# Performance work log

Hardware: AMD Instinct MI355X
Metric: run time of the kernel (lower is better)

The kernel has to match this reference:

```python
import jax, jax.numpy as jnp
import numpy as np
from jax import lax

B, N0, N1 = 4, 256, 256
NVOX = N0 * N1
NSUB, NLOR, RAYLEN, NTOF = 8, 32768, 256, 1
NBLK, CH = 4, 16
SUBSETS = np.linspace(0, NSUB, NBLK, endpoint=False).astype(int)  # [0,2,4,6]


def setup_inputs() -> dict:
    key = jax.random.key(0)
    ks = jax.random.split(key, 12)
    osem = jax.random.uniform(ks[0], (B, 1, N0, N1, 1), jnp.float32) + 0.1
    data = jax.random.uniform(ks[1], (B, NSUB, NLOR, NTOF), jnp.float32)
    mult = jax.random.uniform(ks[2], (B, NSUB, NLOR, 1), jnp.float32) + 0.5
    contam = jax.random.uniform(ks[3], (B, NSUB, NLOR, NTOF), jnp.float32) + 0.1
    adjoint_ones = jax.random.uniform(ks[4], (B, NSUB, N0, N1, 1), jnp.float32) + 0.5
    norm = jax.random.uniform(ks[5], (B,), jnp.float32) + 0.5
    ray_idx = jax.random.randint(ks[6], (NSUB, NLOR, RAYLEN), 0, NVOX, dtype=jnp.int32)
    proj_weights = jax.random.uniform(ks[7], (NSUB, NLOR, RAYLEN), jnp.float32) / RAYLEN
    w1 = jax.random.normal(ks[8], (CH, 1, 3, 3), jnp.float32) * 0.05
    b1 = jnp.zeros((CH,), jnp.float32)
    w2 = jax.random.normal(ks[9], (1, CH, 3, 3), jnp.float32) * 0.05
    b2 = jnp.zeros((1,), jnp.float32)
    net_weight = jnp.asarray(1.0, jnp.float32)
    return dict(osem=osem, data=data, multiplicative_corrections=mult,
                contamination=contam, adjoint_ones=adjoint_ones, norm=norm,
                ray_idx=ray_idx, proj_weights=proj_weights,
                w1=w1, b1=b1, w2=w2, b2=b2, net_weight=net_weight)


def _conv(x, w):
    return lax.conv_general_dilated(x, w, (1, 1), 'SAME',
                                    dimension_numbers=('NCHW', 'OIHW', 'NCHW'))


def _net(x, w1, b1, w2, b2):
    # x: (B,1,N0,N1,1) -> treat as NCHW 2D image with 1 channel
    img = x[:, :, :, :, 0]
    h = jax.nn.relu(_conv(img, w1) + b1[None, :, None, None])
    o = _conv(h, w2) + b2[None, :, None, None]
    return o[..., None]


def _fidelity(x, data, mult, contam, adj_ones, norm, ray_idx, pw, subset):
    # unscaled image, flattened: (B, NVOX)
    img_flat = norm[:, None] * x[:, 0, :, :, 0].reshape(B, NVOX)
    ii = ray_idx[subset]          # (NLOR, RAYLEN) voxel indices per ray
    ww = pw[subset]               # (NLOR, RAYLEN) Joseph weights
    # forward projection: gather + weighted sum along each ray
    fwd = jnp.einsum('bls,ls->bl', img_flat[:, ii], ww)[..., None]  # (B,NLOR,1)
    expected = mult[:, subset] * fwd + contam[:, subset]            # (B,NLOR,NTOF)
    ratio = (mult[:, subset] * (1.0 - data[:, subset] / expected)).sum(-1)  # (B,NLOR)
    # adjoint projection: scatter-add along each ray
    back = jnp.zeros((B, NVOX), x.dtype).at[:, ii].add(ww * ratio[:, :, None])
    upd = back * (img_flat / adj_ones[:, subset].reshape(B, NVOX))
    return (upd / norm[:, None]).reshape(B, 1, N0, N1, 1)


def reference(osem, data, multiplicative_corrections, contamination,
              adjoint_ones, norm, ray_idx, proj_weights,
              w1, b1, w2, b2, net_weight):
    x = osem
    for subset in SUBSETS:
        x_data = _fidelity(x, data, multiplicative_corrections, contamination,
                           adjoint_ones, norm, ray_idx, proj_weights, int(subset))
        x_net = _net(x, w1, b1, w2, b2)
        x = jax.nn.relu(osem - x_data + net_weight * x_net)
    return x
```

## Files before the change

kernel.cpp:

```cpp
#include <hip/hip_runtime.h>
#include <hip/hip_fp16.h>

#define BB 4
#define N0 256
#define N1 256
#define NVOX 65536
#define NSUB 8
#define NLOR 32768
#define RAYLEN 256
#define CH 16
#define NPTS (NLOR * RAYLEN)
#define VOXQ 16384
#define VOXT 32768

__global__ __launch_bounds__(256) void k_transpose(const float* __restrict__ osem,
                                                   float* __restrict__ xt) {
    int v = blockIdx.x * blockDim.x + threadIdx.x;
    if (v >= NVOX) return;
    float4 o;
    o.x = osem[0 * NVOX + v];
    o.y = osem[1 * NVOX + v];
    o.z = osem[2 * NVOX + v];
    o.w = osem[3 * NVOX + v];
    ((float4*)xt)[v] = o;
}

__global__ __launch_bounds__(256) void k_pack(const int* __restrict__ ridx,
                                              const float* __restrict__ pw,
                                              unsigned* __restrict__ packed) {
    int t = blockIdx.x * blockDim.x + threadIdx.x;
    int4   id = ((const int4*)ridx)[t];
    float4 w  = ((const float4*)pw)[t];
    uint4 o;
    o.x = (unsigned)id.x | ((unsigned)__half_as_ushort(__float2half_rn(w.x)) << 16);
    o.y = (unsigned)id.y | ((unsigned)__half_as_ushort(__float2half_rn(w.y)) << 16);
    o.z = (unsigned)id.z | ((unsigned)__half_as_ushort(__float2half_rn(w.z)) << 16);
    o.w = (unsigned)id.w | ((unsigned)__half_as_ushort(__float2half_rn(w.w)) << 16);
    ((uint4*)packed)[t] = o;
}

__device__ __forceinline__ float upk_w(unsigned p) {
    return __half2float(__ushort_as_half((unsigned short)(p >> 16)));
}

__device__ __forceinline__ unsigned pk2(float a, float b) {
    __half2 h = __floats2half2_rn(a, b);
    return *reinterpret_cast<unsigned*>(&h);
}

__global__ __launch_bounds__(256) void k_fwd_p(
    const unsigned* __restrict__ packed,
    const float* __restrict__ xt,
    const float* __restrict__ data,
    const float* __restrict__ mult,
    const float* __restrict__ contam,
    const float* __restrict__ norm,
    float* __restrict__ ratio)
{
    const int wave = threadIdx.x >> 6;
    const int lane = threadIdx.x & 63;
    const int l = blockIdx.x * 4 + wave;

    uint4 P = ((const uint4*)(packed + (size_t)l * RAYLEN))[lane];
    float ax = 0.f, ay = 0.f, az = 0.f, aw = 0.f;
    unsigned pp[4] = {P.x, P.y, P.z, P.w};
#pragma unroll
    for (int k = 0; k < 4; ++k) {
        float wt = upk_w(pp[k]);
        float4 xv = ((const float4*)xt)[pp[k] & 0xffffu];
        ax += xv.x * wt;
        ay += xv.y * wt;
        az += xv.z * wt;
        aw += xv.w * wt;
    }
#pragma unroll
    for (int off = 32; off >= 1; off >>= 1) {
        ax += __shfl_xor(ax, off);
        ay += __shfl_xor(ay, off);
        az += __shfl_xor(az, off);
        aw += __shfl_xor(aw, off);
    }
    if (lane == 0) {
        float fwd[4] = {ax, ay, az, aw};
        float rr[4];
#pragma unroll
        for (int b = 0; b < 4; ++b) {
            long o = (long)b * (NSUB * NLOR) + l;
            float m = mult[o];
            float e = m * (norm[b] * fwd[b]) + contam[o];
            rr[b] = m * (1.0f - data[o] / e);
        }
        ((float4*)ratio)[l] = make_float4(rr[0], rr[1], rr[2], rr[3]);
    }
}

__global__ __launch_bounds__(1024) void k_back_pk(
    const unsigned* __restrict__ packed,
    const float* __restrict__ ratio,
    unsigned* __restrict__ part,
    int PC)
{
    __shared__ unsigned acc[VOXQ];
    const int c = blockIdx.x;
    const int g = blockIdx.y;
    const int p = g & 1;
    const unsigned lo = (unsigned)(g >> 1) * VOXQ;

    for (int q = threadIdx.x; q < VOXQ; q += 1024) acc[q] = 0u;
    __syncthreads();

    const unsigned abase = (unsigned)(uintptr_t)(&acc[0]);

    const int n4 = PC >> 2;
    const uint4* src = (const uint4*)packed + (size_t)c * n4;
    const float2* rat2 = (const float2*)ratio;
    const int e0 = c * n4;

#define PKADD(u, R)                                                              \
    {                                                                            \
        unsigned q_ = ((u) & 0xffffu) - lo;                                      \
        if (q_ < VOXQ) {                                                         \
            float w_ = upk_w(u);                                                 \
            unsigned d_ = pk2(w_ * (R).x, w_ * (R).y);                           \
            unsigned a_ = abase + (q_ << 2);                                     \
            asm volatile("ds_pk_add_f16 %0, %1" :: "v"(a_), "v"(d_) : "memory"); \
        }                                                                        \
    }
#define PROC(P, R) PKADD(P.x, R) PKADD(P.y, R) PKADD(P.z, R) PKADD(P.w, R)

    for (int base4 = 0; base4 < n4; base4 += 4096) {
        const int ea = base4 + (int)threadIdx.x;
        uint4 A = src[ea];
        uint4 B = src[ea + 1024];
        uint4 C2 = src[ea + 2048];
        uint4 D = src[ea + 3072];
        float2 ra = rat2[(((e0 + ea) >> 6) << 1) + p];
        float2 rb = rat2[(((e0 + ea + 1024) >> 6) << 1) + p];
        float2 rc = rat2[(((e0 + ea + 2048) >> 6) << 1) + p];
        float2 rd = rat2[(((e0 + ea + 3072) >> 6) << 1) + p];
        PROC(A, ra) PROC(B, rb) PROC(C2, rc) PROC(D, rd)
    }
#undef PROC
#undef PKADD

    asm volatile("s_waitcnt lgkmcnt(0)" ::: "memory");
    __syncthreads();

    unsigned* dst = part + ((size_t)c * 2 + p) * NVOX + lo;
    for (int q = threadIdx.x; q < VOXQ; q += 1024) dst[q] = acc[q];
}

__global__ __launch_bounds__(256) void k_fwd(
    const int* __restrict__ ridx, const float* __restrict__ pw,
    const float* __restrict__ xt, const float* __restrict__ data,
    const float* __restrict__ mult, const float* __restrict__ contam,
    const float* __restrict__ norm, float* __restrict__ ratio)
{
    const int wave = threadIdx.x >> 6;
    const int lane = threadIdx.x & 63;
    const int l = blockIdx.x * 4 + wave;
    const long base = (long)l * RAYLEN;
    float ax = 0.f, ay = 0.f, az = 0.f, aw = 0.f;
#pragma unroll
    for (int k = 0; k < 4; ++k) {
        int r = lane + (k << 6);
        float wt = pw[base + r];
        float4 xv = ((const float4*)xt)[ridx[base + r]];
        ax += xv.x * wt; ay += xv.y * wt; az += xv.z * wt; aw += xv.w * wt;
    }
#pragma unroll
    for (int off = 32; off >= 1; off >>= 1) {
        ax += __shfl_xor(ax, off); ay += __shfl_xor(ay, off);
        az += __shfl_xor(az, off); aw += __shfl_xor(aw, off);
    }
    if (lane == 0) {
        float fwd[4] = {ax, ay, az, aw};
        float rr[4];
#pragma unroll
        for (int b = 0; b < 4; ++b) {
            long o = (long)b * (NSUB * NLOR) + l;
            float m = mult[o];
            float e = m * (norm[b] * fwd[b]) + contam[o];
            rr[b] = m * (1.0f - data[o] / e);
        }
        ((float4*)ratio)[l] = make_float4(rr[0], rr[1], rr[2], rr[3]);
    }
}

__global__ __launch_bounds__(1024) void k_back(
    const int* __restrict__ ridx, const float* __restrict__ pw,
    const float* __restrict__ ratio, float* __restrict__ part, int PC)
{
    __shared__ float acc[VOXT];
    const int c = blockIdx.x;
    const int g = blockIdx.y;
    const int b = g & 3;
    const int lo = (g >> 2) * VOXT;
    for (int q = threadIdx.x; q < VOXT; q += 1024) acc[q] = 0.0f;
    __syncthreads();
    const int pbeg = c * PC;
    const int pend = min(pbeg + PC, NPTS);
#pragma unroll 2
    for (int pt = pbeg + (int)threadIdx.x * 4; pt < pend; pt += 1024 * 4) {
        int4   id = *(const int4*)(ridx + pt);
        float4 w  = *(const float4*)(pw + pt);
        float  r  = ratio[(pt >> 8) * 4 + b];
        unsigned r0 = (unsigned)(id.x - lo), r1 = (unsigned)(id.y - lo);
        unsigned r2 = (unsigned)(id.z - lo), r3 = (unsigned)(id.w - lo);
        if (r0 < VOXT) atomicAdd(&acc[r0], w.x * r);
        if (r1 < VOXT) atomicAdd(&acc[r1], w.y * r);
        if (r2 < VOXT) atomicAdd(&acc[r2], w.z * r);
        if (r3 < VOXT) atomicAdd(&acc[r3], w.w * r);
    }
    __syncthreads();
    float4* dst = (float4*)(part + ((size_t)c * 4 + b) * NVOX + lo);
    const float4* srcl = (const float4*)acc;
    for (int q = threadIdx.x; q < VOXT / 4; q += 1024) dst[q] = srcl[q];
}

__global__ __launch_bounds__(256) void k_conv1(
    const float* __restrict__ xt,
    const float* __restrict__ w1,
    const float* __restrict__ b1,
    float* __restrict__ h)
{
    int t = blockIdx.x * blockDim.x + threadIdx.x;
    int b = t >> 16;
    int v = t & 65535;
    int i = v >> 8, j = v & 255;
    float in[3][3];
#pragma unroll
    for (int di = 0; di < 3; ++di)
#pragma unroll
        for (int dj = 0; dj < 3; ++dj) {
            int ii = i + di - 1, jj = j + dj - 1;
            in[di][dj] = (ii >= 0 && ii < N0 && jj >= 0 && jj < N1)
                             ? xt[(size_t)((ii << 8) | jj) * 4 + b]
                             : 0.0f;
        }
    float* hp = h + (size_t)t * CH;
#pragma unroll
    for (int c = 0; c < CH; ++c) {
        float acc = b1[c];
#pragma unroll
        for (int di = 0; di < 3; ++di)
#pragma unroll
            for (int dj = 0; dj < 3; ++dj)
                acc += in[di][dj] * w1[c * 9 + di * 3 + dj];
        hp[c] = fmaxf(acc, 0.0f);
    }
}

__global__ __launch_bounds__(256) void k_combine_pk(
    const float* __restrict__ h,
    const float* __restrict__ w2,
    const float* __restrict__ b2,
    const unsigned* __restrict__ part,
    const float* __restrict__ xt_in,
    const float* __restrict__ osem,
    const float* __restrict__ adj,
    const float* __restrict__ nwp,
    int C,
    float* __restrict__ xt_out,
    float* __restrict__ out_planar)
{
    int t = blockIdx.x * blockDim.x + threadIdx.x;
    int b = t >> 16;
    int v = t & 65535;
    int i = v >> 8, j = v & 255;

    float o = b2[0];
#pragma unroll
    for (int di = 0; di < 3; ++di) {
        int ii = i + di - 1;
        if (ii < 0 || ii >= N0) continue;
#pragma unroll
        for (int dj = 0; dj < 3; ++dj) {
            int jj = j + dj - 1;
            if (jj < 0 || jj >= N1) continue;
            const float* hp = h + ((size_t)b * NVOX + ((ii << 8) | jj)) * CH;
#pragma unroll
            for (int c = 0; c < CH; ++c)
                o += hp[c] * w2[c * 9 + di * 3 + dj];
        }
    }
    const int pr = b >> 1, hi = b & 1;
    float bk = 0.0f;
    for (int c = 0; c < C; ++c) {
        unsigned u = part[((size_t)c * 2 + pr) * NVOX + v];
        unsigned short us = hi ? (unsigned short)(u >> 16) : (unsigned short)(u & 0xffffu);
        bk += __half2float(__ushort_as_half(us));
    }

    float xv = xt_in[(size_t)v * 4 + b];
    float x_data = bk * xv / adj[(size_t)b * NSUB * NVOX + v];
    float xnew = osem[t] - x_data + nwp[0] * o;
    xnew = fmaxf(xnew, 0.0f);
    xt_out[(size_t)v * 4 + b] = xnew;
    if (out_planar) out_planar[t] = xnew;
}

__global__ __launch_bounds__(256) void k_combine(
    const float* __restrict__ h, const float* __restrict__ w2,
    const float* __restrict__ b2, const float* __restrict__ part,
    const float* __restrict__ xt_in, const float* __restrict__ osem,
    const float* __restrict__ adj, const float* __restrict__ nwp, int C,
    float* __restrict__ xt_out, float* __restrict__ out_planar)
{
    int t = blockIdx.x * blockDim.x + threadIdx.x;
    int b = t >> 16;
    int v = t & 65535;
    int i = v >> 8, j = v & 255;
    float o = b2[0];
#pragma unroll
    for (int di = 0; di < 3; ++di) {
        int ii = i + di - 1;
        if (ii < 0 || ii >= N0) continue;
#pragma unroll
        for (int dj = 0; dj < 3; ++dj) {
            int jj = j + dj - 1;
            if (jj < 0 || jj >= N1) continue;
            const float* hp = h + ((size_t)b * NVOX + ((ii << 8) | jj)) * CH;
#pragma unroll
            for (int c = 0; c < CH; ++c)
                o += hp[c] * w2[c * 9 + di * 3 + dj];
        }
    }
    float bk = 0.0f;
    for (int c = 0; c < C; ++c)
        bk += part[((size_t)c * 4 + b) * NVOX + v];
    float xv = xt_in[(size_t)v * 4 + b];
    float x_data = bk * xv / adj[(size_t)b * NSUB * NVOX + v];
    float xnew = osem[t] - x_data + nwp[0] * o;
    xnew = fmaxf(xnew, 0.0f);
    xt_out[(size_t)v * 4 + b] = xnew;
    if (out_planar) out_planar[t] = xnew;
}

extern "C" void kernel_launch(void* const* d_in, const int* in_sizes, int n_in,
                              void* d_out, int out_size, void* d_ws, size_t ws_size,
                              hipStream_t stream) {
    const float* osem   = (const float*)d_in[0];
    const float* data   = (const float*)d_in[1];
    const float* mult   = (const float*)d_in[2];
    const float* contam = (const float*)d_in[3];
    const float* adj    = (const float*)d_in[4];
    const float* norm   = (const float*)d_in[5];
    const int*   ray_idx = (const int*)d_in[6];
    const float* pw     = (const float*)d_in[7];
    const float* w1     = (const float*)d_in[8];
    const float* b1     = (const float*)d_in[9];
    const float* w2     = (const float*)d_in[10];
    const float* b2     = (const float*)d_in[11];
    const float* nw     = (const float*)d_in[12];
    float* out = (float*)d_out;

    const size_t MB = 1024 * 1024;
    float* ws  = (float*)d_ws;
    float* xtA = ws;
    float* xtB = ws + (size_t)NVOX * 4;
    const int subsets[4] = {0, 2, 4, 6};

    bool use_pk = (ws_size >= 90 * MB);

    k_transpose<<<NVOX / 256, 256, 0, stream>>>(osem, xtA);

    if (use_pk) {
        const int C = 64;
        const int PC = NPTS / C;
        unsigned* part = (unsigned*)(ws + (size_t)NVOX * 8);
        float* h    = (float*)(part + (size_t)C * 2 * NVOX);
        float* ratio = h;
        unsigned* packed = (unsigned*)(h + (size_t)BB * NVOX * CH);

        float* xin = xtA;
        float* xout = xtB;
        for (int it = 0; it < 4; ++it) {
            int s = subsets[it];
            k_pack<<<NPTS / 4 / 256, 256, 0, stream>>>(
                ray_idx + (size_t)s * NPTS, pw + (size_t)s * NPTS, packed);
            k_fwd_p<<<NLOR / 4, 256, 0, stream>>>(
                packed, xin,
                data + (size_t)s * NLOR, mult + (size_t)s * NLOR,
                contam + (size_t)s * NLOR, norm, ratio);
            k_back_pk<<<dim3(C, 8), 1024, 0, stream>>>(packed, ratio, part, PC);
            k_conv1<<<(BB * NVOX) / 256, 256, 0, stream>>>(xin, w1, b1, h);
            k_combine_pk<<<(BB * NVOX) / 256, 256, 0, stream>>>(
                h, w2, b2, part, xin, osem,
                adj + (size_t)s * NVOX, nw, C,
                xout, (it == 3) ? out : nullptr);
            float* tmp = xin; xin = xout; xout = tmp;
        }
    } else {
        int C = (ws_size >= (18 + 32) * MB + NVOX) ? 32
              : (ws_size >= (18 + 16) * MB + NVOX) ? 16 : 8;
        const int PC = NPTS / C;
        float* part = ws + (size_t)NVOX * 8;
        float* h    = part + (size_t)C * NVOX * 4;
        float* ratio = h;

        float* xin = xtA;
        float* xout = xtB;
        for (int it = 0; it < 4; ++it) {
            int s = subsets[it];
            const int*   rs = ray_idx + (size_t)s * NPTS;
            const float* ps = pw + (size_t)s * NPTS;
            k_fwd<<<NLOR / 4, 256, 0, stream>>>(
                rs, ps, xin,
                data + (size_t)s * NLOR, mult + (size_t)s * NLOR,
                contam + (size_t)s * NLOR, norm, ratio);
            k_back<<<dim3(C, 8), 1024, 0, stream>>>(rs, ps, ratio, part, PC);
            k_conv1<<<(BB * NVOX) / 256, 256, 0, stream>>>(xin, w1, b1, h);
            k_combine<<<(BB * NVOX) / 256, 256, 0, stream>>>(
                h, w2, b2, part, xin, osem,
                adj + (size_t)s * NVOX, nw, C,
                xout, (it == 3) ? out : nullptr);
            float* tmp = xin; xin = xout; xout = tmp;
        }
    }
}
```

Baseline: 760.2 us.

## Fuse packing into forward projection and fuse CNN with combine via shared-memory tiles

Folds the index/weight packing pass into the forward-projection kernel, so the ray data is read once and the packed form is written alongside. It also replaces the separate conv1 kernel and combine kernel with one tiled kernel. That kernel computes the 16-channel hidden layer for a tile plus halo in shared memory and then applies conv2 and the update. This removes two launches per iteration and the global round trip of the large 16-channel hidden tensor. In exchange, halo hidden values are recomputed per tile and the kernel uses about 41 KB of shared memory, which limits occupancy.

```diff
diff --git a/kernel.cpp b/kernel.cpp
--- a/kernel.cpp
+++ b/kernel.cpp
@@ -12,6 +12,7 @@
 #define NPTS (NLOR * RAYLEN)
 #define VOXQ 16384
 #define VOXT 32768
+#define CCH 64
 
 __global__ __launch_bounds__(256) void k_transpose(const float* __restrict__ osem,
                                                    float* __restrict__ xt) {
@@ -25,20 +26,6 @@
     ((float4*)xt)[v] = o;
 }
 
-__global__ __launch_bounds__(256) void k_pack(const int* __restrict__ ridx,
-                                              const float* __restrict__ pw,
-                                              unsigned* __restrict__ packed) {
-    int t = blockIdx.x * blockDim.x + threadIdx.x;
-    int4   id = ((const int4*)ridx)[t];
-    float4 w  = ((const float4*)pw)[t];
-    uint4 o;
-    o.x = (unsigned)id.x | ((unsigned)__half_as_ushort(__float2half_rn(w.x)) << 16);
-    o.y = (unsigned)id.y | ((unsigned)__half_as_ushort(__float2half_rn(w.y)) << 16);
-    o.z = (unsigned)id.z | ((unsigned)__half_as_ushort(__float2half_rn(w.z)) << 16);
-    o.w = (unsigned)id.w | ((unsigned)__half_as_ushort(__float2half_rn(w.w)) << 16);
-    ((uint4*)packed)[t] = o;
-}
-
 __device__ __forceinline__ float upk_w(unsigned p) {
     return __half2float(__ushort_as_half((unsigned short)(p >> 16)));
 }
@@ -48,26 +35,31 @@
     return *reinterpret_cast<unsigned*>(&h);
 }
 
-__global__ __launch_bounds__(256) void k_fwd_p(
-    const unsigned* __restrict__ packed,
+__global__ __launch_bounds__(256) void k_fwdpack(
+    const int* __restrict__ ridx,
+    const float* __restrict__ pw,
     const float* __restrict__ xt,
     const float* __restrict__ data,
     const float* __restrict__ mult,
     const float* __restrict__ contam,
     const float* __restrict__ norm,
-    float* __restrict__ ratio)
+    float* __restrict__ ratio,
+    unsigned* __restrict__ packed)
 {
     const int wave = threadIdx.x >> 6;
     const int lane = threadIdx.x & 63;
     const int l = blockIdx.x * 4 + wave;
-
-    uint4 P = ((const uint4*)(packed + (size_t)l * RAYLEN))[lane];
+    const long base = (long)l * RAYLEN;
+
     float ax = 0.f, ay = 0.f, az = 0.f, aw = 0.f;
-    unsigned pp[4] = {P.x, P.y, P.z, P.w};
 #pragma unroll
     for (int k = 0; k < 4; ++k) {
-        float wt = upk_w(pp[k]);
-        float4 xv = ((const float4*)xt)[pp[k] & 0xffffu];
+        int r = lane + (k << 6);
+        int id = ridx[base + r];
+        float wt = pw[base + r];
+        packed[base + r] = (unsigned)id |
+                           ((unsigned)__half_as_ushort(__float2half_rn(wt)) << 16);
+        float4 xv = ((const float4*)xt)[id];
         ax += xv.x * wt;
         ay += xv.y * wt;
         az += xv.z * wt;
@@ -148,6 +140,93 @@
 
     unsigned* dst = part + ((size_t)c * 2 + p) * NVOX + lo;
     for (int q = threadIdx.x; q < VOXQ; q += 1024) dst[q] = acc[q];
+}
+
+#define TI 16
+#define TJ 32
+__global__ __launch_bounds__(256) void k_net_combine(
+    const float* __restrict__ xt_in,
+    const float* __restrict__ w1,
+    const float* __restrict__ b1,
+    const float* __restrict__ w2,
+    const float* __restrict__ b2,
+    const unsigned* __restrict__ part,
+    const float* __restrict__ osem,
+    const float* __restrict__ adj,
+    const float* __restrict__ nwp,
+    float* __restrict__ xt_out,
+    float* __restrict__ out_planar)
+{
+    __shared__ float img[(TI + 4) * (TJ + 4)];
+    __shared__ float hsm[16 * (TI + 2) * (TJ + 2)];
+    __shared__ float ws1[144], ws2[144], bs1[16];
+
+    const int i0 = blockIdx.x * TI;
+    const int j0 = blockIdx.y * TJ;
+    const int b  = blockIdx.z;
+    const int tid = threadIdx.x;
+
+    if (tid < 144) { ws1[tid] = w1[tid]; ws2[tid] = w2[tid]; }
+    if (tid < 16) bs1[tid] = b1[tid];
+
+    for (int q = tid; q < (TI + 4) * (TJ + 4); q += 256) {
+        int ii = q / (TJ + 4), jj = q % (TJ + 4);
+        int gi = i0 - 2 + ii, gj = j0 - 2 + jj;
+        float v = 0.f;
+        if (gi >= 0 && gi < N0 && gj >= 0 && gj < N1)
+            v = xt_in[(size_t)(gi * N1 + gj) * 4 + b];
+        img[q] = v;
+    }
+    __syncthreads();
+
+    const int HA = (TI + 2) * (TJ + 2);
+    for (int q = tid; q < 16 * HA; q += 256) {
+        int c = q / HA, r = q % HA;
+        int ii = r / (TJ + 2), jj = r % (TJ + 2);
+        int gi = i0 - 1 + ii, gj = j0 - 1 + jj;
+        float hv = 0.f;
+        if (gi >= 0 && gi < N0 && gj >= 0 && gj < N1) {
+            float a = bs1[c];
+#pragma unroll
+            for (int di = 0; di < 3; ++di)
+#pragma unroll
+                for (int dj = 0; dj < 3; ++dj)
+                    a += img[(ii + di) * (TJ + 4) + (jj + dj)] * ws1[c * 9 + di * 3 + dj];
+            hv = fmaxf(a, 0.f);
+        }
+        hsm[q] = hv;
+    }
+    __syncthreads();
+
+    const float nw = nwp[0];
+    const float bb2 = b2[0];
+    const int pr = b >> 1, hi = b & 1;
+    for (int q = tid; q < TI * TJ; q += 256) {
+        int li = q / TJ, lj = q % TJ;
+        int v = (i0 + li) * N1 + (j0 + lj);
+        float o = bb2;
+#pragma unroll
+        for (int c = 0; c < 16; ++c)
+#pragma unroll
+            for (int di = 0; di < 3; ++di)
+#pragma unroll
+                for (int dj = 0; dj < 3; ++dj)
+                    o += hsm[c * HA + (li + di) * (TJ + 2) + (lj + dj)] *
+                         ws2[c * 9 + di * 3 + dj];
+        float bk = 0.f;
+#pragma unroll 8
+        for (int cc = 0; cc < CCH; ++cc) {
+            unsigned u = part[((size_t)cc * 2 + pr) * NVOX + v];
+            unsigned short us = hi ? (unsigned short)(u >> 16)
+                                   : (unsigned short)(u & 0xffffu);
+            bk += __half2float(__ushort_as_half(us));
+        }
+        float xv = xt_in[(size_t)v * 4 + b];
+        float x_data = bk * xv / adj[(size_t)b * NSUB * NVOX + v];
+        float xnew = fmaxf(osem[(size_t)b * NVOX + v] - x_data + nw * o, 0.f);
+        xt_out[(size_t)v * 4 + b] = xnew;
+        if (out_planar) out_planar[(size_t)b * NVOX + v] = xnew;
+    }
 }
 
 __global__ __launch_bounds__(256) void k_fwd(
@@ -219,10 +298,8 @@
 }
 
 __global__ __launch_bounds__(256) void k_conv1(
-    const float* __restrict__ xt,
-    const float* __restrict__ w1,
-    const float* __restrict__ b1,
-    float* __restrict__ h)
+    const float* __restrict__ xt, const float* __restrict__ w1,
+    const float* __restrict__ b1, float* __restrict__ h)
 {
     int t = blockIdx.x * blockDim.x + threadIdx.x;
     int b = t >> 16;
@@ -249,55 +326,6 @@
                 acc += in[di][dj] * w1[c * 9 + di * 3 + dj];
         hp[c] = fmaxf(acc, 0.0f);
     }
-}
-
-__global__ __launch_bounds__(256) void k_combine_pk(
-    const float* __restrict__ h,
-    const float* __restrict__ w2,
-    const float* __restrict__ b2,
-    const unsigned* __restrict__ part,
-    const float* __restrict__ xt_in,
-    const float* __restrict__ osem,
-    const float* __restrict__ adj,
-    const float* __restrict__ nwp,
-    int C,
-    float* __restrict__ xt_out,
-    float* __restrict__ out_planar)
-{
-    int t = blockIdx.x * blockDim.x + threadIdx.x;
-    int b = t >> 16;
-    int v = t & 65535;
-    int i = v >> 8, j = v & 255;
-
-    float o = b2[0];
-#pragma unroll
-    for (int di = 0; di < 3; ++di) {
-        int ii = i + di - 1;
-        if (ii < 0 || ii >= N0) continue;
-#pragma unroll
-        for (int dj = 0; dj < 3; ++dj) {
-            int jj = j + dj - 1;
-            if (jj < 0 || jj >= N1) continue;
-            const float* hp = h + ((size_t)b * NVOX + ((ii << 8) | jj)) * CH;
-#pragma unroll
-            for (int c = 0; c < CH; ++c)
-                o += hp[c] * w2[c * 9 + di * 3 + dj];
-        }
-    }
-    const int pr = b >> 1, hi = b & 1;
-    float bk = 0.0f;
-    for (int c = 0; c < C; ++c) {
-        unsigned u = part[((size_t)c * 2 + pr) * NVOX + v];
-        unsigned short us = hi ? (unsigned short)(u >> 16) : (unsigned short)(u & 0xffffu);
-        bk += __half2float(__ushort_as_half(us));
-    }
-
-    float xv = xt_in[(size_t)v * 4 + b];
-    float x_data = bk * xv / adj[(size_t)b * NSUB * NVOX + v];
-    float xnew = osem[t] - x_data + nwp[0] * o;
-    xnew = fmaxf(xnew, 0.0f);
-    xt_out[(size_t)v * 4 + b] = xnew;
-    if (out_planar) out_planar[t] = xnew;
 }
 
 __global__ __launch_bounds__(256) void k_combine(
@@ -366,28 +394,23 @@
     k_transpose<<<NVOX / 256, 256, 0, stream>>>(osem, xtA);
 
     if (use_pk) {
-        const int C = 64;
-        const int PC = NPTS / C;
-        unsigned* part = (unsigned*)(ws + (size_t)NVOX * 8);
-        float* h    = (float*)(part + (size_t)C * 2 * NVOX);
-        float* ratio = h;
-        unsigned* packed = (unsigned*)(h + (size_t)BB * NVOX * CH);
+        const int PC = NPTS / CCH;
+        unsigned* part   = (unsigned*)(ws + (size_t)NVOX * 8);
+        unsigned* packed = part + (size_t)CCH * 2 * NVOX;
+        float*    ratio  = (float*)(packed + (size_t)NPTS);
 
         float* xin = xtA;
         float* xout = xtB;
         for (int it = 0; it < 4; ++it) {
             int s = subsets[it];
-            k_pack<<<NPTS / 4 / 256, 256, 0, stream>>>(
-                ray_idx + (size_t)s * NPTS, pw + (size_t)s * NPTS, packed);
-            k_fwd_p<<<NLOR / 4, 256, 0, stream>>>(
-                packed, xin,
+            k_fwdpack<<<NLOR / 4, 256, 0, stream>>>(
+                ray_idx + (size_t)s * NPTS, pw + (size_t)s * NPTS, xin,
                 data + (size_t)s * NLOR, mult + (size_t)s * NLOR,
-                contam + (size_t)s * NLOR, norm, ratio);
-            k_back_pk<<<dim3(C, 8), 1024, 0, stream>>>(packed, ratio, part, PC);
-            k_conv1<<<(BB * NVOX) / 256, 256, 0, stream>>>(xin, w1, b1, h);
-            k_combine_pk<<<(BB * NVOX) / 256, 256, 0, stream>>>(
-                h, w2, b2, part, xin, osem,
-                adj + (size_t)s * NVOX, nw, C,
+                contam + (size_t)s * NLOR, norm, ratio, packed);
+            k_back_pk<<<dim3(CCH, 8), 1024, 0, stream>>>(packed, ratio, part, PC);
+            k_net_combine<<<dim3(N0 / TI, N1 / TJ, BB), 256, 0, stream>>>(
+                xin, w1, b1, w2, b2, part, osem,
+                adj + (size_t)s * NVOX, nw,
                 xout, (it == 3) ? out : nullptr);
             float* tmp = xin; xin = xout; xout = tmp;
         }
```

Result: slower. 924.7 us (+21.6%).
